# Performance work log

Hardware: AMD Instinct MI355X
Metric: run time of the kernel (lower is better)

## Reference

```python
import jax, jax.numpy as jnp
import numpy as np
from jax import lax

B, N, D, H, HD = 2, 2048, 2048, 16, 128
EPS = 1e-6


def setup_inputs() -> dict:
    key = jax.random.key(0)
    ks = jax.random.split(key, 6)
    x = jax.random.normal(ks[0], (B, N, D), jnp.float32)
    past_kv = jnp.zeros((B, H, HD, HD), jnp.float32)
    # positive per-head decay slopes, like MiniMax's ALiBi-style slope_rate
    slope_rate = jax.random.uniform(ks[1], (H, 1, 1), jnp.float32, 0.001, 0.1)
    w_qkv = jax.random.normal(ks[2], (3 * H * HD, D), jnp.float32) * 0.02
    w_gate = jax.random.normal(ks[3], (H * HD, D), jnp.float32) * 0.02
    w_out = jax.random.normal(ks[4], (D, H * HD), jnp.float32) * 0.02
    norm_w = jnp.ones((H * HD,), jnp.float32)
    return {"x": x, "past_kv": past_kv, "slope_rate": slope_rate,
            "w_qkv": w_qkv, "w_gate": w_gate, "w_out": w_out, "norm_w": norm_w}


def reference(x, past_kv, slope_rate, w_qkv, w_gate, w_out, norm_w):
    b, n, d = x.shape
    h = slope_rate.shape[0]
    hd = past_kv.shape[-1]

    # qkv projection + silu activation
    qkv = jax.nn.silu(x @ w_qkv.T)                 # [b, n, 3*h*hd]
    qkv = qkv.reshape(b, n, h, 3 * hd)
    q, k, v = jnp.split(qkv, 3, axis=-1)           # each [b, n, h, hd]
    # time-major for scan: [n, b, h, hd]
    q = jnp.transpose(q, (1, 0, 2, 3))
    k = jnp.transpose(k, (1, 0, 2, 3))
    v = jnp.transpose(v, (1, 0, 2, 3))

    ratio = jnp.exp(-slope_rate)                   # [h, 1, 1] broadcasts vs kv [b, h, hd, hd]

    def step(kv, qkv_t):
        q_t, k_t, v_t = qkv_t                      # each [b, h, hd]
        kv = ratio * kv + k_t[..., :, None] * v_t[..., None, :]   # [b, h, dk, dv]
        o = jnp.einsum('bhe,bhed->bhd', q_t, kv)   # contract over k-dim
        return kv, o

    kv_final, out = lax.scan(step, past_kv, (q, k, v))   # out: [n, b, h, hd]
    out = jnp.transpose(out, (1, 0, 2, 3)).reshape(b, n, h * hd)

    # RMSNorm over h*hd (computed in fp32 as in the original)
    var = jnp.mean(out * out, axis=-1, keepdims=True)
    out = norm_w * (out * lax.rsqrt(var + EPS))

    # sigmoid output gate + final projection
    gate = jax.nn.sigmoid(x @ w_gate.T)            # [b, n, h*hd]
    out = (gate * out) @ w_out.T                   # [b, n, d]
    return out, kv_final
```

## Files before the change

### kernel.cpp

```cpp
#include <hip/hip_runtime.h>


typedef __attribute__((ext_vector_type(8))) short short8;
typedef __attribute__((ext_vector_type(4))) float f32x4;

__device__ __forceinline__ float blo(unsigned int u){ return __uint_as_float(u << 16); }
__device__ __forceinline__ float bhi(unsigned int u){ return __uint_as_float(u & 0xffff0000u); }
__device__ __forceinline__ unsigned short f2b(float f){
  unsigned int u = __float_as_uint(f);
  return (unsigned short)((u + 0x7fffu + ((u >> 16) & 1u)) >> 16);
}
__device__ __forceinline__ unsigned int pk2(float a, float b){
  return (unsigned int)f2b(a) | ((unsigned int)f2b(b) << 16);
}

#define GLOAD_LDS16(g, l) __builtin_amdgcn_global_load_lds( \
    (const __attribute__((address_space(1))) unsigned int*)(g), \
    (__attribute__((address_space(3))) unsigned int*)(l), 16, 0, 0)

#define FRAG(buf, row, kt) (*(const short8*)&(buf)[(((row) << 7)) + \
    ((((((kt) << 2) + lk)) ^ ((row) & 15)) << 3)])

#define OFF_XB     ((size_t)0)
#define OFF_WQKVB  ((size_t)16777216)
#define OFF_WGATEB ((size_t)41943040)
#define OFF_WOUTB  ((size_t)50331648)
#define OFF_QB     ((size_t)58720256)
#define OFF_KB     ((size_t)75497472)
#define OFF_VTB    ((size_t)92274688)
#define OFF_KVC    ((size_t)109051904)
#define OFF_ATTN   ((size_t)142606336)
#define OFF_GATE   ((size_t)176160768)
#define OFF_YBUF   ((size_t)192937984)
#define WS_NEED    ((size_t)209715200)

__global__ __launch_bounds__(256)
void cast_f2b(const float* __restrict__ in, unsigned short* __restrict__ o, int n)
{
  int idx = (blockIdx.x * 256 + threadIdx.x) * 4;
  if (idx >= n) return;
  float4 v = *(const float4*)&in[idx];
  ushort4 u;
  u.x = f2b(v.x); u.y = f2b(v.y); u.z = f2b(v.z); u.w = f2b(v.w);
  *(ushort4*)&o[idx] = u;
}

__global__ __launch_bounds__(512, 2)
void gemm256_qkvg(const unsigned short* __restrict__ A, const unsigned short* __restrict__ Bm,
                  const float* __restrict__ slope,
                  unsigned short* __restrict__ qo, unsigned short* __restrict__ ko,
                  unsigned short* __restrict__ vo, unsigned short* __restrict__ go)
{
  __shared__ unsigned short lds[65536];
  const int tid = threadIdx.x, lane = tid & 63, w = tid >> 6;
  const int wm = w >> 2, wn = w & 3;
  const int lr = lane & 15, kg = lane >> 4;

  const int bid = blockIdx.x;
  const int swz = ((bid & 7) << 6) + (bid >> 3);
  const int mBase = (swz >> 5) << 8;
  const int nBase = (swz & 31) << 8;

  auto stage = [&](const unsigned short* __restrict__ src, int rowBase, int k0,
                   unsigned short* lb, int half) {
#pragma unroll
    for (int s = 0; s < 2; ++s) {
      const int idx = (s << 9) + tid;
      const int r = idx >> 3, sl = idx & 7;
      GLOAD_LDS16(src + (size_t)(rowBase + (half << 7) + r) * 2048 + k0
                      + ((sl ^ (r & 7)) << 3),
                  lb + (half << 13) + (((s << 9) + (w << 6)) << 3));
    }
  };

  f32x4 acc[8][4];
#pragma unroll
  for (int m = 0; m < 8; ++m)
#pragma unroll
    for (int n = 0; n < 4; ++n) acc[m][n] = (f32x4){0.f, 0.f, 0.f, 0.f};

  const int NT = 32;
  stage(A,  mBase, 0, lds,        0);
  stage(A,  mBase, 0, lds,        1);
  stage(Bm, nBase, 0, lds + 16384, 0);
  stage(Bm, nBase, 0, lds + 16384, 1);
  __syncthreads();

  for (int t = 0; t < NT; ++t) {
    unsigned short* Ab = lds + ((t & 1) << 15);
    unsigned short* Bb = Ab + 16384;
    unsigned short* An = lds + (((t & 1) ^ 1) << 15);
    unsigned short* Bn = An + 16384;
    const int k0n = (t + 1) << 6;
#pragma unroll
    for (int p = 0; p < 4; ++p) {
      if (t + 1 < NT) {
        if      (p == 0) stage(A,  mBase, k0n, An, 0);
        else if (p == 1) stage(A,  mBase, k0n, An, 1);
        else if (p == 2) stage(Bm, nBase, k0n, Bn, 0);
        else             stage(Bm, nBase, k0n, Bn, 1);
      }
      const int mh = p >> 1, nh = p & 1;
      short8 af[4][2], bf[2][2];
#pragma unroll
      for (int m = 0; m < 4; ++m) {
        const int rA = (wm << 7) + (mh << 6) + (m << 4) + lr;
#pragma unroll
        for (int ks = 0; ks < 2; ++ks)
          af[m][ks] = *(const short8*)&Ab[(rA << 6) + ((((ks << 2) + kg) ^ (rA & 7)) << 3)];
      }
#pragma unroll
      for (int n = 0; n < 2; ++n) {
        const int rB = (wn << 6) + (nh << 5) + (n << 4) + lr;
#pragma unroll
        for (int ks = 0; ks < 2; ++ks)
          bf[n][ks] = *(const short8*)&Bb[(rB << 6) + ((((ks << 2) + kg) ^ (rB & 7)) << 3)];
      }
      __builtin_amdgcn_s_setprio(1);
#pragma unroll
      for (int m = 0; m < 4; ++m)
#pragma unroll
        for (int n = 0; n < 2; ++n)
#pragma unroll
          for (int ks = 0; ks < 2; ++ks)
            acc[(mh << 2) + m][(nh << 1) + n] =
              __builtin_amdgcn_mfma_f32_16x16x32_bf16(af[m][ks], bf[n][ks],
                  acc[(mh << 2) + m][(nh << 1) + n], 0, 0, 0);
      __builtin_amdgcn_s_setprio(0);
      if (p < 3) __builtin_amdgcn_s_barrier();
    }
    __syncthreads();
  }

  const int cb = nBase + (wn << 6);
  const int rowW = mBase + (wm << 7);
  if (cb >= 6144) {
#pragma unroll
    for (int mi = 0; mi < 8; ++mi)
#pragma unroll
      for (int ni = 0; ni < 4; ++ni) {
        f32x4 v = acc[mi][ni];
        const int colg = cb - 6144 + (ni << 4) + lr;
#pragma unroll
        for (int r2 = 0; r2 < 4; ++r2) {
          const int row = rowW + (mi << 4) + (kg << 2) + r2;
          go[((size_t)row << 11) + colg] = f2b(1.f / (1.f + __expf(-v[r2])));
        }
      }
  } else {
    const int hh = cb / 384;
    const int rem = cb - hh * 384;
    const int sub = rem >> 7;
    const int db = rem & 127;
    unsigned short* dst = (sub == 0) ? qo : (sub == 1) ? ko : vo;
#pragma unroll
    for (int mi = 0; mi < 8; ++mi)
#pragma unroll
      for (int ni = 0; ni < 4; ++ni) {
        f32x4 v = acc[mi][ni];
        const int dd = db + (ni << 4) + lr;
#pragma unroll
        for (int r2 = 0; r2 < 4; ++r2) {
          const int row = rowW + (mi << 4) + (kg << 2) + r2;
          const int bb = row >> 11, nn = row & 2047;
          float sv = v[r2] / (1.f + __expf(-v[r2]));
          dst[(((size_t)((bb << 4) + hh) << 11) + nn) * 128 + dd] = f2b(sv);
        }
      }
  }
}

__global__ __launch_bounds__(256)
void tkv(const unsigned short* __restrict__ kg_, const unsigned short* __restrict__ vg_,
         const float* __restrict__ slope, unsigned short* __restrict__ kto,
         unsigned short* __restrict__ vto)
{
  __shared__ unsigned int T[8192];
  __shared__ float lamt[128];
  const int blk = blockIdx.x;
  const int h = (blk >> 4) & 15;
  const int tid = threadIdx.x;
  const size_t base = (size_t)blk << 14;
  if (tid < 128) lamt[tid] = __expf(-slope[h] * (float)(127 - tid));
#pragma unroll
  for (int pass = 0; pass < 2; ++pass) {
    const unsigned short* src = pass ? vg_ : kg_;
    __syncthreads();
#pragma unroll
    for (int it = 0; it < 4; ++it) {
      const int j = ((tid >> 4) << 1) + (it << 5);
      const int d0 = (tid & 15) << 3;
      uint4 a  = *(const uint4*)&src[base + (size_t)j * 128 + d0];
      uint4 b2 = *(const uint4*)&src[base + (size_t)(j + 1) * 128 + d0];
      const unsigned short* ap = (const unsigned short*)&a;
      const unsigned short* bp = (const unsigned short*)&b2;
      const int jp = j >> 1;
#pragma unroll
      for (int t2 = 0; t2 < 8; ++t2) {
        const int d = d0 + t2;
        T[(d << 6) + (jp ^ (((d >> 3) & 15) << 2))] =
            (unsigned int)ap[t2] | ((unsigned int)bp[t2] << 16);
      }
    }
    __syncthreads();
#pragma unroll
    for (int it = 0; it < 8; ++it) {
      const int d = (tid >> 4) + (it << 4);
      const int jp0 = (tid & 15) << 2;
      uint4 u = *(const uint4*)&T[(d << 6) + (jp0 ^ (((d >> 3) & 15) << 2))];
      const int j0 = jp0 << 1;
      if (pass == 0) {
        u.x = pk2(blo(u.x) * lamt[j0],     bhi(u.x) * lamt[j0 + 1]);
        u.y = pk2(blo(u.y) * lamt[j0 + 2], bhi(u.y) * lamt[j0 + 3]);
        u.z = pk2(blo(u.z) * lamt[j0 + 4], bhi(u.z) * lamt[j0 + 5]);
        u.w = pk2(blo(u.w) * lamt[j0 + 6], bhi(u.w) * lamt[j0 + 7]);
        *(uint4*)&kto[base + ((size_t)d << 7) + j0] = u;
      } else {
        *(uint4*)&vto[base + ((size_t)d << 7) + j0] = u;
      }
    }
  }
}

__global__ __launch_bounds__(256)
void gemm_out(const unsigned short* __restrict__ A, const unsigned short* __restrict__ Bm,
              int K, int Nn, float* __restrict__ o0)
{
  __shared__ unsigned short As[4096];
  __shared__ unsigned short Bs[4096];
  const int tid  = threadIdx.x;
  const int lane = tid & 63, w = tid >> 6;
  const int mBase = blockIdx.y << 7, nBase = blockIdx.x << 7;
  f32x4 acc[4][4];
#pragma unroll
  for (int m = 0; m < 4; ++m)
#pragma unroll
    for (int n = 0; n < 4; ++n) acc[m][n] = (f32x4){0.f,0.f,0.f,0.f};
  const int wr = w >> 1, wc = w & 1;
  const int rA = (wr << 6) + (lane & 15);
  const int cB = (wc << 6) + (lane & 15);
  const int kg = (lane >> 4) << 3;
  const int segBase = w << 7;
  const int nIter = K >> 5;
  for (int kt = 0; kt < nIter; ++kt) {
    const int k0 = kt << 5;
#pragma unroll
    for (int rep = 0; rep < 2; ++rep) {
      int seg = segBase + (rep << 6) + lane;
      int r  = seg >> 2;
      int c8 = (seg & 3) << 3;
      GLOAD_LDS16(A  + ((size_t)(mBase + r) * K + k0 + c8), &As[(segBase + (rep << 6)) << 3]);
      GLOAD_LDS16(Bm + ((size_t)(nBase + r) * K + k0 + c8), &Bs[(segBase + (rep << 6)) << 3]);
    }
    __syncthreads();
    short8 af[4], bfv[4];
#pragma unroll
    for (int m = 0; m < 4; ++m) af[m]  = *(const short8*)&As[((rA + (m << 4)) << 5) + kg];
#pragma unroll
    for (int n = 0; n < 4; ++n) bfv[n] = *(const short8*)&Bs[((cB + (n << 4)) << 5) + kg];
#pragma unroll
    for (int m = 0; m < 4; ++m)
#pragma unroll
      for (int n = 0; n < 4; ++n)
        acc[m][n] = __builtin_amdgcn_mfma_f32_16x16x32_bf16(af[m], bfv[n], acc[m][n], 0, 0, 0);
    __syncthreads();
  }
#pragma unroll
  for (int m = 0; m < 4; ++m)
#pragma unroll
    for (int n = 0; n < 4; ++n) {
      const int row0 = mBase + (wr << 6) + (m << 4) + ((lane >> 4) << 2);
      const int col  = nBase + (wc << 6) + (n << 4) + (lane & 15);
      f32x4 v = acc[m][n];
#pragma unroll
      for (int r2 = 0; r2 < 4; ++r2)
        o0[(size_t)(row0 + r2) * Nn + col] = v[r2];
    }
}

__global__ __launch_bounds__(256, 2)
void chunk_kv_mfma(const unsigned short* __restrict__ vtg,
                   const unsigned short* __restrict__ ktg,
                   float* __restrict__ KVc)
{
  __shared__ unsigned short VTs[16384], KTs[16384];
  const int blk = blockIdx.x;
  const int tid = threadIdx.x, lane = tid & 63, w = tid >> 6;
  const int wr = w >> 1, wc = w & 1, lr = lane & 15, lk = lane >> 4;
  const size_t base = (size_t)blk << 14;
#pragma unroll
  for (int it = 0; it < 8; ++it) {
    int segw = (w << 3) + it;
    int sg = (segw << 6) + lane;
    int r = sg >> 4, sl = sg & 15;
    size_t goff = ((size_t)r << 7) + (size_t)((sl ^ (r & 15)) << 3);
    GLOAD_LDS16(vtg + base + goff, &VTs[segw << 9]);
    GLOAD_LDS16(ktg + base + goff, &KTs[segw << 9]);
  }
  __syncthreads();
  f32x4 acc[4][4];
#pragma unroll
  for (int m = 0; m < 4; ++m)
#pragma unroll
    for (int n = 0; n < 4; ++n) acc[m][n] = (f32x4){0.f,0.f,0.f,0.f};
#pragma unroll
  for (int kt = 0; kt < 4; ++kt) {
    short8 af[4], bf2[4];
#pragma unroll
    for (int m = 0; m < 4; ++m) af[m]  = FRAG(VTs, (wr << 6) + (m << 4) + lr, kt);
#pragma unroll
    for (int n = 0; n < 4; ++n) bf2[n] = FRAG(KTs, (wc << 6) + (n << 4) + lr, kt);
#pragma unroll
    for (int m = 0; m < 4; ++m)
#pragma unroll
      for (int n = 0; n < 4; ++n)
        acc[m][n] = __builtin_amdgcn_mfma_f32_16x16x32_bf16(af[m], bf2[n], acc[m][n], 0, 0, 0);
  }
  float* outp = KVc + base;
#pragma unroll
  for (int m = 0; m < 4; ++m)
#pragma unroll
    for (int n = 0; n < 4; ++n)
#pragma unroll
      for (int r2 = 0; r2 < 4; ++r2)
        outp[(size_t)((wr << 6) + (m << 4) + (lk << 2) + r2) * 128
             + (wc << 6) + (n << 4) + lr] = acc[m][n][r2];
}

__global__ __launch_bounds__(256)
void combine_kv(float* __restrict__ KVc, const float* __restrict__ past_kv,
                const float* __restrict__ slope, float* __restrict__ outkv)
{
  const int bh = blockIdx.x >> 3, slice = blockIdx.x & 7;
  const int h = bh & 15;
  const int tid = threadIdx.x;
  const float lamC = __expf(-slope[h] * 128.f);
  const int f0 = (slice << 11) + tid;
  float S[8];
  const float* pp = past_kv + ((size_t)bh << 14);
#pragma unroll
  for (int i = 0; i < 8; ++i) {
    int f = f0 + (i << 8);
    int d = f >> 7, e = f & 127;
    S[i] = pp[(e << 7) + d];
  }
  for (int cc = 0; cc < 16; ++cc) {
    float* p = KVc + ((((size_t)bh << 4) + cc) << 14);
#pragma unroll
    for (int i = 0; i < 8; ++i) {
      int f = f0 + (i << 8);
      float t = p[f];
      p[f] = S[i];
      S[i] = lamC * S[i] + t;
    }
  }
  float* op = outkv + ((size_t)bh << 14);
#pragma unroll
  for (int i = 0; i < 8; ++i) {
    int f = f0 + (i << 8);
    int d = f >> 7, e = f & 127;
    op[(e << 7) + d] = S[i];
  }
}

__global__ __launch_bounds__(256, 1)
void chunk_out_mfma(const unsigned short* __restrict__ qg,
                    const unsigned short* __restrict__ kg,
                    const unsigned short* __restrict__ vtg,
                    const float* __restrict__ States,
                    const float* __restrict__ slope,
                    float* __restrict__ attn)
{
  __shared__ unsigned short Qs[16384], Ks[16384], VTs[16384], STs[16384];
  const int blk = blockIdx.x;
  const int cc = blk & 15, h = (blk >> 4) & 15, b = blk >> 8;
  const int tid = threadIdx.x, lane = tid & 63, w = tid >> 6;
  const int wr = w >> 1, wc = w & 1, lr = lane & 15, lk = lane >> 4;
  const size_t base = (size_t)blk << 14;
  const float s = slope[h];
#pragma unroll
  for (int it = 0; it < 8; ++it) {
    int segw = (w << 3) + it;
    int sg = (segw << 6) + lane;
    int r = sg >> 4, sl = sg & 15;
    size_t goff = ((size_t)r << 7) + (size_t)((sl ^ (r & 15)) << 3);
    GLOAD_LDS16(qg  + base + goff, &Qs[segw << 9]);
    GLOAD_LDS16(kg  + base + goff, &Ks[segw << 9]);
    GLOAD_LDS16(vtg + base + goff, &VTs[segw << 9]);
  }
  const float* Sg = States + base;
#pragma unroll
  for (int it = 0; it < 8; ++it) {
    int idx = ((it << 8) + tid) << 3;
    float4 a0 = *(const float4*)&Sg[idx];
    float4 a1 = *(const float4*)&Sg[idx + 4];
    int r = idx >> 7, c = idx & 127;
    int sl = (c >> 3) ^ (r & 15);
    uint4 u = make_uint4(pk2(a0.x,a0.y), pk2(a0.z,a0.w), pk2(a1.x,a1.y), pk2(a1.z,a1.w));
    *(uint4*)&STs[(r << 7) + (sl << 3)] = u;
  }
  __syncthreads();

  f32x4 Oa[4][4], Pa[4][4];
#pragma unroll
  for (int m = 0; m < 4; ++m)
#pragma unroll
    for (int n = 0; n < 4; ++n) { Oa[m][n] = (f32x4){0.f,0.f,0.f,0.f}; Pa[m][n] = (f32x4){0.f,0.f,0.f,0.f}; }

#pragma unroll
  for (int kt = 0; kt < 4; ++kt) {
    short8 qf[4], bst[4], bk[4];
#pragma unroll
    for (int m = 0; m < 4; ++m) qf[m] = FRAG(Qs, (wr << 6) + (m << 4) + lr, kt);
#pragma unroll
    for (int n = 0; n < 4; ++n) {
      int cn = (wc << 6) + (n << 4) + lr;
      bst[n] = FRAG(STs, cn, kt);
      bk[n]  = FRAG(Ks,  cn, kt);
    }
#pragma unroll
    for (int m = 0; m < 4; ++m)
#pragma unroll
      for (int n = 0; n < 4; ++n) {
        Oa[m][n] = __builtin_amdgcn_mfma_f32_16x16x32_bf16(qf[m], bst[n], Oa[m][n], 0, 0, 0);
        Pa[m][n] = __builtin_amdgcn_mfma_f32_16x16x32_bf16(qf[m], bk[n],  Pa[m][n], 0, 0, 0);
      }
  }

  float emi[16];
#pragma unroll
  for (int m = 0; m < 4; ++m)
#pragma unroll
    for (int r2 = 0; r2 < 4; ++r2)
      emi[(m << 2) + r2] = __expf(-s * (float)((wr << 6) + (m << 4) + (lk << 2) + r2));
  const float lam1 = __expf(-s);
  float epj[4];
#pragma unroll
  for (int n = 0; n < 4; ++n)
    epj[n] = __expf(s * (float)((wc << 6) + (n << 4) + lr));

#pragma unroll
  for (int m = 0; m < 4; ++m)
#pragma unroll
    for (int n = 0; n < 4; ++n) {
      const int j = (wc << 6) + (n << 4) + lr;
#pragma unroll
      for (int r2 = 0; r2 < 4; ++r2) {
        const int i = (wr << 6) + (m << 4) + (lk << 2) + r2;
        Oa[m][n][r2] *= emi[(m << 2) + r2] * lam1;
        float pv = Pa[m][n][r2] * emi[(m << 2) + r2] * epj[n];
        Pa[m][n][r2] = (i >= j) ? pv : 0.f;
      }
    }
  __syncthreads();

#pragma unroll
  for (int m = 0; m < 4; ++m)
#pragma unroll
    for (int n = 0; n < 4; ++n) {
      const int j = (wc << 6) + (n << 4) + lr;
#pragma unroll
      for (int r2 = 0; r2 < 4; ++r2) {
        const int i = (wr << 6) + (m << 4) + (lk << 2) + r2;
        const int sl = (j >> 3) ^ (i & 15);
        Ks[(i << 7) + (sl << 3) + (j & 7)] = f2b(Pa[m][n][r2]);
      }
    }
  __syncthreads();

#pragma unroll
  for (int kt = 0; kt < 4; ++kt) {
    short8 pf[4], vf[4];
#pragma unroll
    for (int m = 0; m < 4; ++m) pf[m] = FRAG(Ks,  (wr << 6) + (m << 4) + lr, kt);
#pragma unroll
    for (int n = 0; n < 4; ++n) vf[n] = FRAG(VTs, (wc << 6) + (n << 4) + lr, kt);
#pragma unroll
    for (int m = 0; m < 4; ++m)
#pragma unroll
      for (int n = 0; n < 4; ++n)
        Oa[m][n] = __builtin_amdgcn_mfma_f32_16x16x32_bf16(pf[m], vf[n], Oa[m][n], 0, 0, 0);
  }

#pragma unroll
  for (int m = 0; m < 4; ++m)
#pragma unroll
    for (int n = 0; n < 4; ++n) {
      const int c = (wc << 6) + (n << 4) + lr;
#pragma unroll
      for (int r2 = 0; r2 < 4; ++r2) {
        const int i = (wr << 6) + (m << 4) + (lk << 2) + r2;
        attn[(((size_t)((b << 11) + (cc << 7) + i)) << 11) + (h << 7) + c] = Oa[m][n][r2];
      }
    }
}

__global__ __launch_bounds__(256)
void norm_gate(const float* __restrict__ attn, const unsigned short* __restrict__ gateb,
               const float* __restrict__ normw, unsigned short* __restrict__ ybuf)
{
  const int row = blockIdx.x;
  const int tid = threadIdx.x;
  const float* ar = attn + ((size_t)row << 11);
  float4 v0 = *(const float4*)&ar[tid * 8];
  float4 v1 = *(const float4*)&ar[tid * 8 + 4];
  float ss = v0.x*v0.x + v0.y*v0.y + v0.z*v0.z + v0.w*v0.w
           + v1.x*v1.x + v1.y*v1.y + v1.z*v1.z + v1.w*v1.w;
#pragma unroll
  for (int off = 32; off > 0; off >>= 1) ss += __shfl_down(ss, off);
  __shared__ float red[4];
  if ((tid & 63) == 0) red[tid >> 6] = ss;
  __syncthreads();
  float tot = red[0] + red[1] + red[2] + red[3];
  float scale = rsqrtf(tot * (1.f / 2048.f) + 1e-6f);
  uint4 gg = *(const uint4*)&gateb[((size_t)row << 11) + tid * 8];
  float4 w0 = *(const float4*)&normw[tid * 8];
  float4 w1 = *(const float4*)&normw[tid * 8 + 4];
  ushort4 o0, o1;
  o0.x = f2b(v0.x * scale * w0.x * blo(gg.x));
  o0.y = f2b(v0.y * scale * w0.y * bhi(gg.x));
  o0.z = f2b(v0.z * scale * w0.z * blo(gg.y));
  o0.w = f2b(v0.w * scale * w0.w * bhi(gg.y));
  o1.x = f2b(v1.x * scale * w1.x * blo(gg.z));
  o1.y = f2b(v1.y * scale * w1.y * bhi(gg.z));
  o1.z = f2b(v1.z * scale * w1.z * blo(gg.w));
  o1.w = f2b(v1.w * scale * w1.w * bhi(gg.w));
  *(ushort4*)&ybuf[((size_t)row << 11) + tid * 8]     = o0;
  *(ushort4*)&ybuf[((size_t)row << 11) + tid * 8 + 4] = o1;
}

extern "C" void kernel_launch(void* const* d_in, const int* in_sizes, int n_in,
                              void* d_out, int out_size, void* d_ws, size_t ws_size,
                              hipStream_t stream)
{
  const float* x       = (const float*)d_in[0];
  const float* past_kv = (const float*)d_in[1];
  const float* slope   = (const float*)d_in[2];
  const float* w_qkv   = (const float*)d_in[3];
  const float* w_gate  = (const float*)d_in[4];
  const float* w_out   = (const float*)d_in[5];
  const float* norm_w  = (const float*)d_in[6];
  float* out    = (float*)d_out;
  float* out_kv = out + 8388608;
  if (ws_size < WS_NEED) return;
  char* ws = (char*)d_ws;
  unsigned short* xb     = (unsigned short*)(ws + OFF_XB);
  unsigned short* wqkvb  = (unsigned short*)(ws + OFF_WQKVB);
  unsigned short* wgateb = (unsigned short*)(ws + OFF_WGATEB);
  unsigned short* woutb  = (unsigned short*)(ws + OFF_WOUTB);
  unsigned short* qb     = (unsigned short*)(ws + OFF_QB);
  unsigned short* kb     = (unsigned short*)(ws + OFF_KB);
  unsigned short* vtb    = (unsigned short*)(ws + OFF_VTB);
  unsigned short* vrow   = (unsigned short*)(ws + OFF_ATTN);
  unsigned short* ktb    = (unsigned short*)(ws + OFF_YBUF);
  float*          kvc    = (float*)(ws + OFF_KVC);
  float*          attn   = (float*)(ws + OFF_ATTN);
  unsigned short* gate   = (unsigned short*)(ws + OFF_GATE);
  unsigned short* ybuf   = (unsigned short*)(ws + OFF_YBUF);

  cast_f2b<<<8192,  256, 0, stream>>>(x,      xb,     8388608);
  cast_f2b<<<12288, 256, 0, stream>>>(w_qkv,  wqkvb,  12582912);
  cast_f2b<<<4096,  256, 0, stream>>>(w_gate, wgateb, 4194304);
  cast_f2b<<<4096,  256, 0, stream>>>(w_out,  woutb,  4194304);

  gemm256_qkvg<<<512, 512, 0, stream>>>(xb, wqkvb, slope, qb, kb, vrow, gate);

  tkv<<<512, 256, 0, stream>>>(kb, vrow, slope, ktb, vtb);

  chunk_kv_mfma <<<512, 256, 0, stream>>>(vtb, ktb, kvc);
  combine_kv    <<<256, 256, 0, stream>>>(kvc, past_kv, slope, out_kv);
  chunk_out_mfma<<<512, 256, 0, stream>>>(qb, kb, vtb, kvc, slope, attn);

  norm_gate<<<4096, 256, 0, stream>>>(attn, gate, norm_w, ybuf);
  gemm_out<<<dim3(16, 32), 256, 0, stream>>>(ybuf, woutb, 2048, 2048, out);
}
```

Before: 429.1 us.

## Restructure QKV-gate GEMM main loop with fine-grained vmcnt waits and fragment reuse

Rewrites the 256x256 bf16 GEMM main loop into a four-phase schedule. Explicit s_waitcnt vmcnt counters plus bare s_barrier replace the per-iteration __syncthreads, and the loads for the next k-tile are interleaved with MFMA work on the current tile. Warp-to-subtile mapping changes so A and B fragments are reused across quadrants, which cuts LDS reads. Block-to-tile swizzling is also changed for L2 locality. Hand-tuned waitcnt values risk races if the count of in-flight global-to-LDS loads does not match.

```diff
diff --git a/kernel.cpp b/kernel.cpp
--- a/kernel.cpp
+++ b/kernel.cpp
@@ -17,6 +17,9 @@
 #define GLOAD_LDS16(g, l) __builtin_amdgcn_global_load_lds( \
     (const __attribute__((address_space(1))) unsigned int*)(g), \
     (__attribute__((address_space(3))) unsigned int*)(l), 16, 0, 0)
+
+#define VMCNT(N) asm volatile("s_waitcnt vmcnt(" #N ")" ::: "memory")
+#define SBAR()   __builtin_amdgcn_s_barrier()
 
 #define FRAG(buf, row, kt) (*(const short8*)&(buf)[(((row) << 7)) + \
     ((((((kt) << 2) + lk)) ^ ((row) & 15)) << 3)])
@@ -57,16 +60,17 @@
   const int lr = lane & 15, kg = lane >> 4;
 
   const int bid = blockIdx.x;
-  const int swz = ((bid & 7) << 6) + (bid >> 3);
-  const int mBase = (swz >> 5) << 8;
-  const int nBase = (swz & 31) << 8;
+  const int x = bid & 7, idx0 = bid >> 3;
+  const int mt = ((x >> 2) << 3) + (idx0 >> 3);
+  const int nt = ((x & 3) << 3) + (idx0 & 7);
+  const int mBase = mt << 8, nBase = nt << 8;
 
   auto stage = [&](const unsigned short* __restrict__ src, int rowBase, int k0,
                    unsigned short* lb, int half) {
 #pragma unroll
     for (int s = 0; s < 2; ++s) {
-      const int idx = (s << 9) + tid;
-      const int r = idx >> 3, sl = idx & 7;
+      const int idx2 = (s << 9) + tid;
+      const int r = idx2 >> 3, sl = idx2 & 7;
       GLOAD_LDS16(src + (size_t)(rowBase + (half << 7) + r) * 2048 + k0
                       + ((sl ^ (r & 7)) << 3),
                   lb + (half << 13) + (((s << 9) + (w << 6)) << 3));
@@ -79,94 +83,125 @@
 #pragma unroll
     for (int n = 0; n < 4; ++n) acc[m][n] = (f32x4){0.f, 0.f, 0.f, 0.f};
 
+  auto loadA = [&](short8 af[4][2], const unsigned short* Ab, int a) {
+#pragma unroll
+    for (int m = 0; m < 4; ++m) {
+      const int rA = (a << 7) + (wm << 6) + (m << 4) + lr;
+#pragma unroll
+      for (int ks = 0; ks < 2; ++ks)
+        af[m][ks] = *(const short8*)&Ab[(rA << 6) + ((((ks << 2) + kg) ^ (rA & 7)) << 3)];
+    }
+  };
+  auto loadB = [&](short8 bf[2][2], const unsigned short* Bb, int b) {
+#pragma unroll
+    for (int n = 0; n < 2; ++n) {
+      const int rB = (b << 7) + (wn << 5) + (n << 4) + lr;
+#pragma unroll
+      for (int ks = 0; ks < 2; ++ks)
+        bf[n][ks] = *(const short8*)&Bb[(rB << 6) + ((((ks << 2) + kg) ^ (rB & 7)) << 3)];
+    }
+  };
+  auto mfma8 = [&](short8 af[4][2], short8 bf[2][2], int a, int b) {
+    __builtin_amdgcn_s_setprio(1);
+#pragma unroll
+    for (int m = 0; m < 4; ++m)
+#pragma unroll
+      for (int n = 0; n < 2; ++n)
+#pragma unroll
+        for (int ks = 0; ks < 2; ++ks)
+          acc[(a << 2) + m][(b << 1) + n] = __builtin_amdgcn_mfma_f32_16x16x32_bf16(
+              af[m][ks], bf[n][ks], acc[(a << 2) + m][(b << 1) + n], 0, 0, 0);
+    __builtin_amdgcn_s_setprio(0);
+  };
+
   const int NT = 32;
-  stage(A,  mBase, 0, lds,        0);
-  stage(A,  mBase, 0, lds,        1);
+  stage(A,  mBase, 0, lds,         0);
   stage(Bm, nBase, 0, lds + 16384, 0);
   stage(Bm, nBase, 0, lds + 16384, 1);
-  __syncthreads();
-
-  for (int t = 0; t < NT; ++t) {
+  stage(A,  mBase, 0, lds,         1);
+
+  for (int t = 0; t < NT - 1; ++t) {
     unsigned short* Ab = lds + ((t & 1) << 15);
     unsigned short* Bb = Ab + 16384;
     unsigned short* An = lds + (((t & 1) ^ 1) << 15);
     unsigned short* Bn = An + 16384;
     const int k0n = (t + 1) << 6;
-#pragma unroll
-    for (int p = 0; p < 4; ++p) {
-      if (t + 1 < NT) {
-        if      (p == 0) stage(A,  mBase, k0n, An, 0);
-        else if (p == 1) stage(A,  mBase, k0n, An, 1);
-        else if (p == 2) stage(Bm, nBase, k0n, Bn, 0);
-        else             stage(Bm, nBase, k0n, Bn, 1);
-      }
-      const int mh = p >> 1, nh = p & 1;
-      short8 af[4][2], bf[2][2];
-#pragma unroll
-      for (int m = 0; m < 4; ++m) {
-        const int rA = (wm << 7) + (mh << 6) + (m << 4) + lr;
-#pragma unroll
-        for (int ks = 0; ks < 2; ++ks)
-          af[m][ks] = *(const short8*)&Ab[(rA << 6) + ((((ks << 2) + kg) ^ (rA & 7)) << 3)];
-      }
-#pragma unroll
-      for (int n = 0; n < 2; ++n) {
-        const int rB = (wn << 6) + (nh << 5) + (n << 4) + lr;
-#pragma unroll
-        for (int ks = 0; ks < 2; ++ks)
-          bf[n][ks] = *(const short8*)&Bb[(rB << 6) + ((((ks << 2) + kg) ^ (rB & 7)) << 3)];
-      }
-      __builtin_amdgcn_s_setprio(1);
-#pragma unroll
-      for (int m = 0; m < 4; ++m)
-#pragma unroll
-        for (int n = 0; n < 2; ++n)
-#pragma unroll
-          for (int ks = 0; ks < 2; ++ks)
-            acc[(mh << 2) + m][(nh << 1) + n] =
-              __builtin_amdgcn_mfma_f32_16x16x32_bf16(af[m][ks], bf[n][ks],
-                  acc[(mh << 2) + m][(nh << 1) + n], 0, 0, 0);
-      __builtin_amdgcn_s_setprio(0);
-      if (p < 3) __builtin_amdgcn_s_barrier();
-    }
-    __syncthreads();
-  }
-
-  const int cb = nBase + (wn << 6);
-  const int rowW = mBase + (wm << 7);
-  if (cb >= 6144) {
-#pragma unroll
-    for (int mi = 0; mi < 8; ++mi)
-#pragma unroll
-      for (int ni = 0; ni < 4; ++ni) {
-        f32x4 v = acc[mi][ni];
-        const int colg = cb - 6144 + (ni << 4) + lr;
-#pragma unroll
-        for (int r2 = 0; r2 < 4; ++r2) {
-          const int row = rowW + (mi << 4) + (kg << 2) + r2;
-          go[((size_t)row << 11) + colg] = f2b(1.f / (1.f + __expf(-v[r2])));
-        }
-      }
-  } else {
-    const int hh = cb / 384;
-    const int rem = cb - hh * 384;
-    const int sub = rem >> 7;
-    const int db = rem & 127;
-    unsigned short* dst = (sub == 0) ? qo : (sub == 1) ? ko : vo;
-#pragma unroll
-    for (int mi = 0; mi < 8; ++mi)
-#pragma unroll
-      for (int ni = 0; ni < 4; ++ni) {
-        f32x4 v = acc[mi][ni];
-        const int dd = db + (ni << 4) + lr;
-#pragma unroll
-        for (int r2 = 0; r2 < 4; ++r2) {
-          const int row = rowW + (mi << 4) + (kg << 2) + r2;
-          const int bb = row >> 11, nn = row & 2047;
-          float sv = v[r2] / (1.f + __expf(-v[r2]));
-          dst[(((size_t)((bb << 4) + hh) << 11) + nn) * 128 + dd] = f2b(sv);
-        }
-      }
+    short8 af[4][2], bf0[2][2], bf1[2][2];
+    VMCNT(4); SBAR();
+    loadA(af, Ab, 0); loadB(bf0, Bb, 0);
+    stage(A, mBase, k0n, An, 0);
+    mfma8(af, bf0, 0, 0);
+    VMCNT(4); SBAR();
+    loadB(bf1, Bb, 1);
+    stage(Bm, nBase, k0n, Bn, 0);
+    mfma8(af, bf1, 0, 1);
+    VMCNT(4); SBAR();
+    loadA(af, Ab, 1);
+    stage(Bm, nBase, k0n, Bn, 1);
+    mfma8(af, bf1, 1, 1);
+    SBAR();
+    stage(A, mBase, k0n, An, 1);
+    mfma8(af, bf0, 1, 0);
+  }
+  {
+    unsigned short* Ab = lds + (((NT - 1) & 1) << 15);
+    unsigned short* Bb = Ab + 16384;
+    short8 af[4][2], bf0[2][2], bf1[2][2];
+    VMCNT(4); SBAR();
+    loadA(af, Ab, 0); loadB(bf0, Bb, 0);
+    mfma8(af, bf0, 0, 0);
+    VMCNT(2); SBAR();
+    loadB(bf1, Bb, 1);
+    mfma8(af, bf1, 0, 1);
+    VMCNT(0); SBAR();
+    loadA(af, Ab, 1);
+    mfma8(af, bf1, 1, 1);
+    SBAR();
+    mfma8(af, bf0, 1, 0);
+  }
+
+#pragma unroll
+  for (int b2 = 0; b2 < 2; ++b2) {
+    const int cb = nBase + (b2 << 7);
+    if (cb >= 6144) {
+      const int colg0 = cb - 6144 + (wn << 5);
+#pragma unroll
+      for (int a = 0; a < 2; ++a)
+#pragma unroll
+        for (int m = 0; m < 4; ++m)
+#pragma unroll
+          for (int n = 0; n < 2; ++n) {
+            f32x4 v = acc[(a << 2) + m][(b2 << 1) + n];
+            const int col = colg0 + (n << 4) + lr;
+#pragma unroll
+            for (int r2 = 0; r2 < 4; ++r2) {
+              const int row = mBase + (a << 7) + (wm << 6) + (m << 4) + (kg << 2) + r2;
+              go[((size_t)row << 11) + col] = f2b(1.f / (1.f + __expf(-v[r2])));
+            }
+          }
+    } else {
+      const int hh = cb / 384;
+      const int rem = cb - hh * 384;
+      const int sub = rem >> 7;
+      const int db = (rem & 127) + (wn << 5);
+      unsigned short* dst = (sub == 0) ? qo : (sub == 1) ? ko : vo;
+#pragma unroll
+      for (int a = 0; a < 2; ++a)
+#pragma unroll
+        for (int m = 0; m < 4; ++m)
+#pragma unroll
+          for (int n = 0; n < 2; ++n) {
+            f32x4 v = acc[(a << 2) + m][(b2 << 1) + n];
+            const int dd = db + (n << 4) + lr;
+#pragma unroll
+            for (int r2 = 0; r2 < 4; ++r2) {
+              const int row = mBase + (a << 7) + (wm << 6) + (m << 4) + (kg << 2) + r2;
+              const int bb = row >> 11, nn = row & 2047;
+              float sv = v[r2] / (1.f + __expf(-v[r2]));
+              dst[(((size_t)((bb << 4) + hh) << 11) + nn) * 128 + dd] = f2b(sv);
+            }
+          }
+    }
   }
 }
 
```

Result: faster. 419.4 us (-2.3%).
